# Performance work log

Measured on AMD Instinct MI355X. Metric: run time of the kernel, lower is better.

Reference implementation:

```python
import jax, jax.numpy as jnp
import numpy as np

B, S = 4, 128
N_ITERS = 3  # original hardcodes range(3) regardless of max_iter


def _build_masks(edge_mask, chart_mask):
    S_ = edge_mask.shape[-1]
    ar = jnp.arange(S_)
    ne = ar[:, None] != ar[None, :]          # [a,b]: a != b
    le = ar[:, None] <= ar[None, :]
    ge = ar[:, None] >= ar[None, :]
    ls = jnp.minimum(ar[:, None], ar[None, :])  # min(a,b)
    rs = jnp.maximum(ar[:, None], ar[None, :])  # max(a,b)

    # edge_mask2o[b,h,m,s] = edge_mask[b,h,s] & edge_mask[b,h,m] & (m != s)
    em2o = edge_mask[:, :, None, :] & edge_mask[:, :, :, None]
    em2o = em2o & ne[None, None, :, :]
    # lrhs[h,m,s] = (min(m,s) >= h) | (max(m,s) <= h)
    lrhs = (ls[None, :, :] >= ar[:, None, None]) | (rs[None, :, :] <= ar[:, None, None])
    noncross = em2o & lrhs[None]
    # additionally require h != s for plain edge_mask2o
    em2o = em2o & ne[:, None, :][None]

    cm0 = chart_mask[:, 0]                                  # [B,S]
    pad = cm0[:, :, None] & cm0[:, None, :]                 # [B,S,S]
    chart_r = jnp.roll(chart_mask, 1, axis=1)               # cat((cm[:,-1:], cm[:,:-1]))
    # span_mask2o[b,i,j,s] = chart_r[b,i,j] & pad[b,j,s] & (max(i,j) != s)
    span2o = chart_r[:, :, :, None] & pad[:, None, :, :]
    span2o = span2o & (rs[:, :, None] != ar[None, None, :])[None]
    # inside[i,j,s] = (i <= s) & (j >= s)
    inside = le[:, None, :] & ge[None, :, :]
    outside = (~inside)[None] & span2o
    # off-diagonal pad mask: pad.triu(1) | pad.tril(-1) == pad & (i != j)
    outside = outside & (pad & ne[None])[:, :, :, None]
    return em2o, noncross, span2o, outside


def setup_inputs() -> dict:
    key = jax.random.key(0)
    ks = jax.random.split(key, 12)
    lens = jax.random.randint(ks[0], (B,), S // 2, S)
    valid = jnp.arange(S)[None, :] < lens[:, None]          # [B,S]
    edge_mask = valid[:, :, None] & valid[:, None, :]
    tri = jnp.triu(jnp.ones((S, S), dtype=bool), 1)
    chart_mask = edge_mask & tri[None]
    def rn(k, shape):
        return jax.random.normal(k, shape, dtype=jnp.float32)
    return {
        's_edge': rn(ks[1], (B, S, S)),
        's_const': rn(ks[2], (B, S, S)),
        's_sib': rn(ks[3], (B, S, S, S)),
        's_cop': rn(ks[4], (B, S, S, S)),
        's_grd': rn(ks[5], (B, S, S, S)),
        's_end_point': rn(ks[6], (B, S, S, S)),
        's_split': rn(ks[7], (B, S, S, S)),
        's_head_span_b': rn(ks[8], (B, S, S, S)),
        's_head_span_e': rn(ks[9], (B, S, S, S)),
        'edge_mask': edge_mask,
        'chart_mask': chart_mask,
    }


def reference(s_edge, s_const, s_sib, s_cop, s_grd, s_end_point, s_split,
              s_head_span_b, s_head_span_e, edge_mask, chart_mask):
    # symmetrize span scores: triu + triu(1).T on last two dims
    s_span = jnp.triu(s_const) + jnp.swapaxes(jnp.triu(s_const, 1), -1, -2)
    em2o, noncross, span2o, outside = _build_masks(edge_mask, chart_mask)

    s_sib = s_sib * em2o
    s_cop = s_cop * em2o
    s_grd = s_grd * em2o
    s_end_point = s_end_point * noncross
    s_split = s_split * span2o
    s_hb = s_head_span_b * outside
    s_he = jnp.transpose(s_head_span_e, (0, 2, 1, 3)) * outside

    # Note: the torch code aliases tmp_q_edge to s_edge and uses +=, so the
    # base scores accumulate across iterations; equivalently q <- q + update.
    q_edge, q_span = s_edge, s_span
    for _ in range(N_ITERS):
        pe = jax.nn.sigmoid(q_edge)
        ps = jax.nn.sigmoid(q_span)
        upd_e = (jnp.einsum('bhs,bhms->bhm', pe, s_sib)
                 + jnp.einsum('bsm,bhms->bhm', pe, s_cop)
                 + jnp.einsum('bms,bhms->bhm', ps, s_grd)
                 + jnp.einsum('bms,bhms->bhm', ps, s_end_point))
        upd_s = (jnp.einsum('bis,bijs->bis', ps, s_split)
                 + jnp.einsum('bsi,bijs->bij', pe, s_hb)
                 + jnp.einsum('bsj,bijs->bij', pe, s_he))
        q_edge = q_edge + upd_e
        q_span = q_span + upd_s
    return q_edge, q_span
```

## Files before the change

kernel.cpp:

```cpp
#include <hip/hip_runtime.h>
#include <stdint.h>

#define BB 4
#define SDIM 128
#define S2 (SDIM*SDIM)
#define S3 ((size_t)SDIM*S2)

__device__ __forceinline__ int probe_len(const void* em, int b, int lane) {
    const unsigned char* p8 = (const unsigned char*)em;
    const int* p32 = (const int*)em;
    const int t0 = lane, t1 = lane + 64;
    const size_t i0 = (size_t)b*S2 + (size_t)t0*SDIM + t0;
    const size_t i1 = (size_t)b*S2 + (size_t)t1*SDIM + t1;
    const unsigned char a0 = p8[i0], a1 = p8[i1];
    const bool ok = (a0 != 0) && (t1 != SDIM-1 || a1 == 0);
    const unsigned long long mok = __ballot(ok);
    const bool use8 = (mok == ~0ull);
    int v0, v1;
    if (use8) { v0 = (a0 != 0); v1 = (a1 != 0); }
    else      { v0 = (p32[i0] != 0); v1 = (p32[i1] != 0); }
    return __popcll(__ballot(v0)) + __popcll(__ballot(v1));
}

__device__ __forceinline__ float sigf(float x) { return 1.f / (1.f + expf(-x)); }

__global__ __launch_bounds__(256) void k_prep(
    const float* __restrict__ s_edge, const float* __restrict__ s_const,
    const float* __restrict__ s_split, const void* __restrict__ em,
    float* __restrict__ q_edge, float* __restrict__ q_span,
    float* __restrict__ split0, float* __restrict__ split1,
    float* __restrict__ peA, float* __restrict__ peB,
    float* __restrict__ peTA, float* __restrict__ peTB,
    float* __restrict__ psA, float* __restrict__ psB) {
    const int b = blockIdx.x >> 7, i = blockIdx.x & 127;
    const int y = blockIdx.y;
    const int tid = threadIdx.x, lane = tid & 63;
    const int len = probe_len(em, b, lane);
    const int lm1 = len - 1;
    const size_t vb = (size_t)b*S2;
    if (y == 0 && tid < SDIM) {
        const size_t ro = vb + (size_t)i*SDIM + tid;
        const float qe = s_edge[ro];
        const float qs = (i <= tid) ? s_const[ro] : s_const[vb + (size_t)tid*SDIM + i];
        q_edge[ro] = qe;
        q_span[ro] = qs;
        const float se = sigf(qe), ss = sigf(qs);
        peA[ro] = se; peB[ro] = se;
        psA[ro] = ss; psB[ro] = ss;
        const size_t to = vb + (size_t)tid*SDIM + i;
        peTA[to] = se; peTB[to] = se;
    }
    const int g = tid >> 5;
    const int kq = (tid & 31) * 4;
    float4 acc = make_float4(0.f, 0.f, 0.f, 0.f);
    if (i >= 1 && i < len && kq < len) {
        const float* base = s_split + (size_t)b*S3 + (size_t)i*S2;
        const int j0 = i + g + 8*y;
        float4 v[8]; int jv[8];
        #pragma unroll
        for (int t = 0; t < 8; ++t) {
            const int j = j0 + 16*t;
            jv[t] = j;
            const int jc = min(j, lm1);
            v[t] = *(const float4*)(base + (size_t)jc*SDIM + kq);
        }
        __builtin_amdgcn_sched_barrier(0);
        #pragma unroll
        for (int t = 0; t < 8; ++t) {
            const int j = jv[t];
            const bool jb = (j < len);
            acc.x += (jb && j != kq+0) ? v[t].x : 0.f;
            acc.y += (jb && j != kq+1) ? v[t].y : 0.f;
            acc.z += (jb && j != kq+2) ? v[t].z : 0.f;
            acc.w += (jb && j != kq+3) ? v[t].w : 0.f;
        }
    }
    __shared__ float red[8][SDIM];
    *(float4*)&red[g][kq] = acc;
    __syncthreads();
    if (tid < SDIM) {
        float s = 0.f;
        #pragma unroll
        for (int gg = 0; gg < 8; ++gg) s += red[gg][tid];
        float* out = y ? split1 : split0;
        out[vb + (size_t)i*SDIM + tid] = (tid >= 1 && tid < len) ? s : 0.f;
    }
}

__global__ __launch_bounds__(256) void k_upd(
    const float* __restrict__ s_sib, const float* __restrict__ s_cop,
    const float* __restrict__ s_grd, const float* __restrict__ s_ep,
    const float* __restrict__ s_hb,  const float* __restrict__ s_he,
    const float* __restrict__ peA, const float* __restrict__ peTA,
    const float* __restrict__ psA,
    const float* __restrict__ split0, const float* __restrict__ split1,
    const void* __restrict__ em,
    float* __restrict__ q_edge, float* __restrict__ q_span,
    float* __restrict__ peB, float* __restrict__ peTB, float* __restrict__ psB) {
    const int b = blockIdx.x >> 7, row = blockIdx.x & 127;
    const int tid = threadIdx.x, wave = tid >> 6, lane = tid & 63;
    const int half = lane >> 5, sq = (lane & 31) * 4;
    const int len = probe_len(em, b, lane);
    const int lm1 = len - 1;
    const int sqa = min(sq, lm1 & ~3);
    const size_t vb = (size_t)b*S2;

    if (blockIdx.y < 4) {
        const int h = row;
        if (h >= len) return;
        const int m0 = blockIdx.y * 32;
        if (m0 >= len) return;
        const size_t tb = (size_t)b*S3 + (size_t)h*S2;
        const size_t hrow = vb + (size_t)h*SDIM;
        const float4 pe4 = *(const float4*)(peA + hrow + sqa);
        int   mr[4];
        float4 sib[4], cop[4], grd[4], epv[4], pet[4], psv[4];
        float qo[4];
        #pragma unroll
        for (int it = 0; it < 4; ++it) {
            const int m = m0 + 8*it + 2*wave + half;
            mr[it] = m;
            const int mc = min(m, lm1);
            const size_t ro = tb + (size_t)mc*SDIM + sqa;
            sib[it] = *(const float4*)(s_sib + ro);
            cop[it] = *(const float4*)(s_cop + ro);
            grd[it] = *(const float4*)(s_grd + ro);
            epv[it] = *(const float4*)(s_ep  + ro);
            const size_t vo = vb + (size_t)mc*SDIM + sqa;
            pet[it] = *(const float4*)(peTA + vo);
            psv[it] = *(const float4*)(psA  + vo);
            qo[it]  = q_edge[hrow + mc];
        }
        __builtin_amdgcn_sched_barrier(0);
        #pragma unroll
        for (int it = 0; it < 4; ++it) {
            const int m = mr[it];
            const bool mv = (m < len);
            float r = 0.f;
            #define TERM(C, F) { const int s = sq + C;                               \
                const bool bs = mv && (s < len) && (m != s);                         \
                const float fem = (bs && (h != s)) ? 1.f : 0.f;                      \
                const float fnc = (bs && ((m >= h && s >= h) || (m <= h && s <= h))) \
                                  ? 1.f : 0.f;                                       \
                r += fem * (sib[it].F*pe4.F + cop[it].F*pet[it].F + grd[it].F*psv[it].F) \
                   + fnc * (epv[it].F*psv[it].F); }
            TERM(0, x) TERM(1, y) TERM(2, z) TERM(3, w)
            #undef TERM
            r += __shfl_xor(r, 16); r += __shfl_xor(r, 8); r += __shfl_xor(r, 4);
            r += __shfl_xor(r, 2);  r += __shfl_xor(r, 1);
            if ((lane & 31) == 0 && mv) {
                const float qn = qo[it] + r;
                q_edge[hrow + m] = qn;
                const float sg = sigf(qn);
                peB[hrow + m] = sg;
                peTB[vb + (size_t)m*SDIM + h] = sg;
            }
        }
    } else {
        const int i = row;
        if (i < 1 || i >= len) return;
        const int j0 = (blockIdx.y - 4) * 32;
        if (j0 >= len) return;
        const size_t irow = vb + (size_t)i*SDIM;
        const float4 peTi4 = *(const float4*)(peTA + irow + sqa);
        int jr[4];
        float4 hb[4], he[4], ptj[4];
        float qs[4], pq[4], s0[4], s1[4];
        #pragma unroll
        for (int it = 0; it < 4; ++it) {
            const int j = j0 + 8*it + 2*wave + half;
            jr[it] = j;
            const int jc = min(j, lm1);
            hb[it]  = *(const float4*)(s_hb + (size_t)b*S3 + (size_t)i*S2 + (size_t)jc*SDIM + sqa);
            he[it]  = *(const float4*)(s_he + (size_t)b*S3 + (size_t)jc*S2 + (size_t)i*SDIM + sqa);
            ptj[it] = *(const float4*)(peTA + vb + (size_t)jc*SDIM + sqa);
            qs[it]  = q_span[irow + jc];
            pq[it]  = psA[irow + jc];
            s0[it]  = split0[irow + jc];
            s1[it]  = split1[irow + jc];
        }
        __builtin_amdgcn_sched_barrier(0);
        #pragma unroll
        for (int it = 0; it < 4; ++it) {
            const int j = jr[it];
            const bool act = (j > i) && (j < len);
            float r = 0.f;
            #define TERM(C, F) { const int s = sq + C;                               \
                const float f = (act && s >= 1 && s < len && (s < i || s > j))       \
                                ? 1.f : 0.f;                                         \
                r += f * (hb[it].F*peTi4.F + he[it].F*ptj[it].F); }
            TERM(0, x) TERM(1, y) TERM(2, z) TERM(3, w)
            #undef TERM
            r += __shfl_xor(r, 16); r += __shfl_xor(r, 8); r += __shfl_xor(r, 4);
            r += __shfl_xor(r, 2);  r += __shfl_xor(r, 1);
            if ((lane & 31) == 0 && j >= 1 && j < len) {
                const float qn = qs[it] + r + pq[it] * (s0[it] + s1[it]);
                q_span[irow + j] = qn;
                psB[irow + j] = sigf(qn);
            }
        }
    }
}

extern "C" void kernel_launch(void* const* d_in, const int* in_sizes, int n_in,
                              void* d_out, int out_size, void* d_ws, size_t ws_size,
                              hipStream_t stream) {
    const float* s_edge  = (const float*)d_in[0];
    const float* s_const = (const float*)d_in[1];
    const float* s_sib   = (const float*)d_in[2];
    const float* s_cop   = (const float*)d_in[3];
    const float* s_grd   = (const float*)d_in[4];
    const float* s_ep    = (const float*)d_in[5];
    const float* s_split = (const float*)d_in[6];
    const float* s_hb    = (const float*)d_in[7];
    const float* s_he    = (const float*)d_in[8];
    const void*  em      = d_in[9];
    (void)in_sizes; (void)n_in; (void)out_size; (void)ws_size;

    float* q_edge = (float*)d_out;
    float* q_span = q_edge + (size_t)BB * S2;

    char* ws = (char*)d_ws;
    const size_t SZ = (size_t)BB * S2 * sizeof(float);
    float* split0 = (float*)(ws);
    float* split1 = (float*)(ws + 1*SZ);
    float* peA    = (float*)(ws + 2*SZ);
    float* peTA   = (float*)(ws + 3*SZ);
    float* psA    = (float*)(ws + 4*SZ);
    float* peB    = (float*)(ws + 5*SZ);
    float* peTB   = (float*)(ws + 6*SZ);
    float* psB    = (float*)(ws + 7*SZ);

    const int NB = BB * SDIM;
    hipLaunchKernelGGL(k_prep, dim3(NB, 2), dim3(256), 0, stream,
                       s_edge, s_const, s_split, em, q_edge, q_span,
                       split0, split1, peA, peB, peTA, peTB, psA, psB);
    for (int it = 0; it < 3; ++it) {
        const int s = it & 1;
        const float* peR  = s ? peB  : peA;
        const float* peTR = s ? peTB : peTA;
        const float* psR  = s ? psB  : psA;
        float* peW  = s ? peA  : peB;
        float* peTW = s ? peTA : peTB;
        float* psW  = s ? psA  : psB;
        hipLaunchKernelGGL(k_upd, dim3(dim3(NB, 8)), dim3(256), 0, stream,
                           s_sib, s_cop, s_grd, s_ep, s_hb, s_he,
                           peR, peTR, psR, split0, split1, em,
                           q_edge, q_span, peW, peTW, psW);
    }
}
```

Before: 278.6 us.

## Stage tensor rows via direct global-to-LDS loads and halve per-block tiles

Both kernels now stream their 3D score rows with global_load_lds (16-byte direct-to-LDS transfers) instead of holding them in register arrays. After a barrier each wave reads its rows from LDS. k_upd processes 16 rows per block instead of 32 and launches twice as many blocks. k_prep stages s_split rows into a 32KB LDS buffer and reduces them column-wise. The aim is to cut register pressure, raise memory-level parallelism and occupancy, and issue loads asynchronously. In exchange it adds barriers and large LDS footprints (48KB in k_upd) that may limit how many blocks fit per CU.

```diff
diff --git a/kernel.cpp b/kernel.cpp
--- a/kernel.cpp
+++ b/kernel.cpp
@@ -24,6 +24,12 @@
 
 __device__ __forceinline__ float sigf(float x) { return 1.f / (1.f + expf(-x)); }
 
+__device__ __forceinline__ void gll16(const float* g, float* l) {
+    __builtin_amdgcn_global_load_lds(
+        (const __attribute__((address_space(1))) void*)g,
+        (__attribute__((address_space(3))) void*)l, 16, 0, 0);
+}
+
 __global__ __launch_bounds__(256) void k_prep(
     const float* __restrict__ s_edge, const float* __restrict__ s_const,
     const float* __restrict__ s_split, const void* __restrict__ em,
@@ -32,9 +38,11 @@
     float* __restrict__ peA, float* __restrict__ peB,
     float* __restrict__ peTA, float* __restrict__ peTB,
     float* __restrict__ psA, float* __restrict__ psB) {
+    __shared__ float plds[64*SDIM];
+    __shared__ float red2[2][SDIM];
     const int b = blockIdx.x >> 7, i = blockIdx.x & 127;
     const int y = blockIdx.y;
-    const int tid = threadIdx.x, lane = tid & 63;
+    const int tid = threadIdx.x, lane = tid & 63, wave = tid >> 6;
     const int len = probe_len(em, b, lane);
     const int lm1 = len - 1;
     const size_t vb = (size_t)b*S2;
@@ -50,40 +58,33 @@
         const size_t to = vb + (size_t)tid*SDIM + i;
         peTA[to] = se; peTB[to] = se;
     }
-    const int g = tid >> 5;
-    const int kq = (tid & 31) * 4;
-    float4 acc = make_float4(0.f, 0.f, 0.f, 0.f);
-    if (i >= 1 && i < len && kq < len) {
-        const float* base = s_split + (size_t)b*S3 + (size_t)i*S2;
-        const int j0 = i + g + 8*y;
-        float4 v[8]; int jv[8];
-        #pragma unroll
-        for (int t = 0; t < 8; ++t) {
-            const int j = j0 + 16*t;
-            jv[t] = j;
+    if (i >= 1 && i < len) {
+        const int L = len - i;
+        const float* sb = s_split + (size_t)b*S3 + (size_t)i*S2;
+        for (int mloc = wave; mloc < 32; mloc += 4) {
+            const int t0 = 2*(y + 2*mloc);
+            if (t0 >= L) break;
+            const int j = i + t0 + (lane >> 5);
             const int jc = min(j, lm1);
-            v[t] = *(const float4*)(base + (size_t)jc*SDIM + kq);
-        }
-        __builtin_amdgcn_sched_barrier(0);
-        #pragma unroll
-        for (int t = 0; t < 8; ++t) {
-            const int j = jv[t];
-            const bool jb = (j < len);
-            acc.x += (jb && j != kq+0) ? v[t].x : 0.f;
-            acc.y += (jb && j != kq+1) ? v[t].y : 0.f;
-            acc.z += (jb && j != kq+2) ? v[t].z : 0.f;
-            acc.w += (jb && j != kq+3) ? v[t].w : 0.f;
-        }
-    }
-    __shared__ float red[8][SDIM];
-    *(float4*)&red[g][kq] = acc;
+            gll16(sb + (size_t)jc*SDIM + (lane & 31)*4, &plds[(2*mloc)*SDIM]);
+        }
+    }
+    __syncthreads();
+    const int k = tid & 127, rh = tid >> 7;
+    float sum = 0.f;
+    #pragma unroll
+    for (int u = 0; u < 32; ++u) {
+        const int r = rh + 2*u;
+        const int j = i + 4*u + 2*y + rh;
+        sum += (j < len && j != k) ? plds[r*SDIM + k] : 0.f;
+    }
+    red2[rh][k] = sum;
     __syncthreads();
     if (tid < SDIM) {
-        float s = 0.f;
-        #pragma unroll
-        for (int gg = 0; gg < 8; ++gg) s += red[gg][tid];
         float* out = y ? split1 : split0;
-        out[vb + (size_t)i*SDIM + tid] = (tid >= 1 && tid < len) ? s : 0.f;
+        out[vb + (size_t)i*SDIM + tid] =
+            (i >= 1 && i < len && tid >= 1 && tid < len)
+            ? (red2[0][tid] + red2[1][tid]) : 0.f;
     }
 }
 
@@ -97,59 +98,62 @@
     const void* __restrict__ em,
     float* __restrict__ q_edge, float* __restrict__ q_span,
     float* __restrict__ peB, float* __restrict__ peTB, float* __restrict__ psB) {
+    __shared__ float lds[6*16*SDIM];
+    __shared__ float sml[64];
     const int b = blockIdx.x >> 7, row = blockIdx.x & 127;
     const int tid = threadIdx.x, wave = tid >> 6, lane = tid & 63;
     const int half = lane >> 5, sq = (lane & 31) * 4;
     const int len = probe_len(em, b, lane);
     const int lm1 = len - 1;
-    const int sqa = min(sq, lm1 & ~3);
     const size_t vb = (size_t)b*S2;
 
-    if (blockIdx.y < 4) {
+    if (blockIdx.y < 8) {
         const int h = row;
-        if (h >= len) return;
-        const int m0 = blockIdx.y * 32;
-        if (m0 >= len) return;
+        const int m0 = blockIdx.y * 16;
+        if (h >= len || m0 >= len) return;
         const size_t tb = (size_t)b*S3 + (size_t)h*S2;
         const size_t hrow = vb + (size_t)h*SDIM;
-        const float4 pe4 = *(const float4*)(peA + hrow + sqa);
-        int   mr[4];
-        float4 sib[4], cop[4], grd[4], epv[4], pet[4], psv[4];
-        float qo[4];
-        #pragma unroll
-        for (int it = 0; it < 4; ++it) {
-            const int m = m0 + 8*it + 2*wave + half;
-            mr[it] = m;
-            const int mc = min(m, lm1);
-            const size_t ro = tb + (size_t)mc*SDIM + sqa;
-            sib[it] = *(const float4*)(s_sib + ro);
-            cop[it] = *(const float4*)(s_cop + ro);
-            grd[it] = *(const float4*)(s_grd + ro);
-            epv[it] = *(const float4*)(s_ep  + ro);
-            const size_t vo = vb + (size_t)mc*SDIM + sqa;
-            pet[it] = *(const float4*)(peTA + vo);
-            psv[it] = *(const float4*)(psA  + vo);
-            qo[it]  = q_edge[hrow + mc];
-        }
-        __builtin_amdgcn_sched_barrier(0);
-        #pragma unroll
-        for (int it = 0; it < 4; ++it) {
-            const int m = mr[it];
+        const float* bases[6] = { s_sib + tb, s_cop + tb, s_grd + tb,
+                                  s_ep + tb,  peTA + vb,  psA + vb };
+        #pragma unroll
+        for (int T = 0; T < 6; ++T) {
+            #pragma unroll
+            for (int ss = 0; ss < 2; ++ss) {
+                const int s  = 2*wave + ss;
+                const int r2 = 2*s + half;
+                const int mc = min(m0 + r2, lm1);
+                gll16(bases[T] + (size_t)mc*SDIM + sq, &lds[(T*16 + 2*s)*SDIM]);
+            }
+        }
+        if (tid < 16)
+            sml[tid] = q_edge[hrow + min(m0 + tid, lm1)];
+        __syncthreads();
+        const float4 pe4 = *(const float4*)(peA + hrow + sq);
+        #pragma unroll
+        for (int it = 0; it < 2; ++it) {
+            const int m = m0 + it*8 + wave*2 + half;
+            const int r = it*8 + wave*2 + half;
+            const float4 sibv = *(const float4*)&lds[(0*16 + r)*SDIM + sq];
+            const float4 copv = *(const float4*)&lds[(1*16 + r)*SDIM + sq];
+            const float4 grdv = *(const float4*)&lds[(2*16 + r)*SDIM + sq];
+            const float4 epvv = *(const float4*)&lds[(3*16 + r)*SDIM + sq];
+            const float4 petv = *(const float4*)&lds[(4*16 + r)*SDIM + sq];
+            const float4 psvv = *(const float4*)&lds[(5*16 + r)*SDIM + sq];
             const bool mv = (m < len);
-            float r = 0.f;
+            float rr = 0.f;
             #define TERM(C, F) { const int s = sq + C;                               \
                 const bool bs = mv && (s < len) && (m != s);                         \
                 const float fem = (bs && (h != s)) ? 1.f : 0.f;                      \
                 const float fnc = (bs && ((m >= h && s >= h) || (m <= h && s <= h))) \
                                   ? 1.f : 0.f;                                       \
-                r += fem * (sib[it].F*pe4.F + cop[it].F*pet[it].F + grd[it].F*psv[it].F) \
-                   + fnc * (epv[it].F*psv[it].F); }
+                rr += fem * (sibv.F*pe4.F + copv.F*petv.F + grdv.F*psvv.F)           \
+                    + fnc * (epvv.F*psvv.F); }
             TERM(0, x) TERM(1, y) TERM(2, z) TERM(3, w)
             #undef TERM
-            r += __shfl_xor(r, 16); r += __shfl_xor(r, 8); r += __shfl_xor(r, 4);
-            r += __shfl_xor(r, 2);  r += __shfl_xor(r, 1);
+            rr += __shfl_xor(rr, 16); rr += __shfl_xor(rr, 8); rr += __shfl_xor(rr, 4);
+            rr += __shfl_xor(rr, 2);  rr += __shfl_xor(rr, 1);
             if ((lane & 31) == 0 && mv) {
-                const float qn = qo[it] + r;
+                const float qn = sml[r] + rr;
                 q_edge[hrow + m] = qn;
                 const float sg = sigf(qn);
                 peB[hrow + m] = sg;
@@ -158,43 +162,51 @@
         }
     } else {
         const int i = row;
-        if (i < 1 || i >= len) return;
-        const int j0 = (blockIdx.y - 4) * 32;
-        if (j0 >= len) return;
+        const int j0 = (blockIdx.y - 8) * 16;
+        if (i < 1 || i >= len || j0 >= len) return;
         const size_t irow = vb + (size_t)i*SDIM;
-        const float4 peTi4 = *(const float4*)(peTA + irow + sqa);
-        int jr[4];
-        float4 hb[4], he[4], ptj[4];
-        float qs[4], pq[4], s0[4], s1[4];
-        #pragma unroll
-        for (int it = 0; it < 4; ++it) {
-            const int j = j0 + 8*it + 2*wave + half;
-            jr[it] = j;
-            const int jc = min(j, lm1);
-            hb[it]  = *(const float4*)(s_hb + (size_t)b*S3 + (size_t)i*S2 + (size_t)jc*SDIM + sqa);
-            he[it]  = *(const float4*)(s_he + (size_t)b*S3 + (size_t)jc*S2 + (size_t)i*SDIM + sqa);
-            ptj[it] = *(const float4*)(peTA + vb + (size_t)jc*SDIM + sqa);
-            qs[it]  = q_span[irow + jc];
-            pq[it]  = psA[irow + jc];
-            s0[it]  = split0[irow + jc];
-            s1[it]  = split1[irow + jc];
-        }
-        __builtin_amdgcn_sched_barrier(0);
-        #pragma unroll
-        for (int it = 0; it < 4; ++it) {
-            const int j = jr[it];
+        #pragma unroll
+        for (int ss = 0; ss < 2; ++ss) {
+            const int s  = 2*wave + ss;
+            const int r2 = 2*s + half;
+            const int jc = min(j0 + r2, lm1);
+            gll16(s_hb + (size_t)b*S3 + (size_t)i*S2 + (size_t)jc*SDIM + sq,
+                  &lds[(0*16 + 2*s)*SDIM]);
+            gll16(s_he + (size_t)b*S3 + (size_t)jc*S2 + (size_t)i*SDIM + sq,
+                  &lds[(1*16 + 2*s)*SDIM]);
+            gll16(peTA + vb + (size_t)jc*SDIM + sq,
+                  &lds[(2*16 + 2*s)*SDIM]);
+        }
+        if (tid < 64) {
+            const int surf = tid >> 4, jj = tid & 15;
+            const int jc = min(j0 + jj, lm1);
+            const size_t o = irow + jc;
+            const float v = (surf == 0) ? q_span[o]
+                          : (surf == 1) ? psA[o]
+                          : (surf == 2) ? split0[o] : split1[o];
+            sml[tid] = v;
+        }
+        __syncthreads();
+        const float4 peTi4 = *(const float4*)(peTA + irow + sq);
+        #pragma unroll
+        for (int it = 0; it < 2; ++it) {
+            const int j = j0 + it*8 + wave*2 + half;
+            const int r = it*8 + wave*2 + half;
+            const float4 hbv  = *(const float4*)&lds[(0*16 + r)*SDIM + sq];
+            const float4 hev  = *(const float4*)&lds[(1*16 + r)*SDIM + sq];
+            const float4 ptjv = *(const float4*)&lds[(2*16 + r)*SDIM + sq];
             const bool act = (j > i) && (j < len);
-            float r = 0.f;
+            float rr = 0.f;
             #define TERM(C, F) { const int s = sq + C;                               \
                 const float f = (act && s >= 1 && s < len && (s < i || s > j))       \
                                 ? 1.f : 0.f;                                         \
-                r += f * (hb[it].F*peTi4.F + he[it].F*ptj[it].F); }
+                rr += f * (hbv.F*peTi4.F + hev.F*ptjv.F); }
             TERM(0, x) TERM(1, y) TERM(2, z) TERM(3, w)
             #undef TERM
-            r += __shfl_xor(r, 16); r += __shfl_xor(r, 8); r += __shfl_xor(r, 4);
-            r += __shfl_xor(r, 2);  r += __shfl_xor(r, 1);
+            rr += __shfl_xor(rr, 16); rr += __shfl_xor(rr, 8); rr += __shfl_xor(rr, 4);
+            rr += __shfl_xor(rr, 2);  rr += __shfl_xor(rr, 1);
             if ((lane & 31) == 0 && j >= 1 && j < len) {
-                const float qn = qs[it] + r + pq[it] * (s0[it] + s1[it]);
+                const float qn = sml[r] + rr + sml[16 + r] * (sml[32 + r] + sml[48 + r]);
                 q_span[irow + j] = qn;
                 psB[irow + j] = sigf(qn);
             }
@@ -243,7 +255,7 @@
         float* peW  = s ? peA  : peB;
         float* peTW = s ? peTA : peTB;
         float* psW  = s ? psA  : psB;
-        hipLaunchKernelGGL(k_upd, dim3(dim3(NB, 8)), dim3(256), 0, stream,
+        hipLaunchKernelGGL(k_upd, dim3(dim3(NB, 16)), dim3(256), 0, stream,
                            s_sib, s_cop, s_grd, s_ep, s_hb, s_he,
                            peR, peTR, psR, split0, split1, em,
                            q_edge, q_span, peW, peTW, psW);
```

Measured after the change: 294.6 us. 1.06x slower.

## Rebalance grids: 4-way split in prep, 64-row chunks per upd block

Applied to the files above, without the earlier changes.

The prep kernel now splits the split-score reduction four ways instead of two. Each block issues fewer loads and accumulates as it goes, replacing the staged register array. The update kernel now has each block process two 32-row sub-chunks sequentially, interleaves edge and span blocks on a flat 1D grid, and sets a minimum occupancy hint of 6 in launch bounds. The aim is to balance work across CUs and improve occupancy, at the cost of less in-flight memory-level parallelism per block, since the sched_barrier batching was removed.

```diff
diff --git a/kernel.cpp b/kernel.cpp
--- a/kernel.cpp
+++ b/kernel.cpp
@@ -5,6 +5,8 @@
 #define SDIM 128
 #define S2 (SDIM*SDIM)
 #define S3 ((size_t)SDIM*S2)
+
+typedef float vf4 __attribute__((ext_vector_type(4)));
 
 __device__ __forceinline__ int probe_len(const void* em, int b, int lane) {
     const unsigned char* p8 = (const unsigned char*)em;
@@ -24,21 +26,23 @@
 
 __device__ __forceinline__ float sigf(float x) { return 1.f / (1.f + expf(-x)); }
 
-__global__ __launch_bounds__(256) void k_prep(
+__global__ __launch_bounds__(256, 6) void k_prep(
     const float* __restrict__ s_edge, const float* __restrict__ s_const,
     const float* __restrict__ s_split, const void* __restrict__ em,
     float* __restrict__ q_edge, float* __restrict__ q_span,
     float* __restrict__ split0, float* __restrict__ split1,
+    float* __restrict__ split2, float* __restrict__ split3,
     float* __restrict__ peA, float* __restrict__ peB,
     float* __restrict__ peTA, float* __restrict__ peTB,
     float* __restrict__ psA, float* __restrict__ psB) {
-    const int b = blockIdx.x >> 7, i = blockIdx.x & 127;
-    const int y = blockIdx.y;
+    const int gid = blockIdx.x;
+    const int yq = gid & 3, x = gid >> 2;
+    const int b = x >> 7, i = x & 127;
     const int tid = threadIdx.x, lane = tid & 63;
     const int len = probe_len(em, b, lane);
     const int lm1 = len - 1;
     const size_t vb = (size_t)b*S2;
-    if (y == 0 && tid < SDIM) {
+    if (yq == 0 && tid < SDIM) {
         const size_t ro = vb + (size_t)i*SDIM + tid;
         const float qe = s_edge[ro];
         const float qs = (i <= tid) ? s_const[ro] : s_const[vb + (size_t)tid*SDIM + i];
@@ -52,52 +56,51 @@
     }
     const int g = tid >> 5;
     const int kq = (tid & 31) * 4;
-    float4 acc = make_float4(0.f, 0.f, 0.f, 0.f);
+    vf4 acc = (vf4)0.f;
     if (i >= 1 && i < len && kq < len) {
         const float* base = s_split + (size_t)b*S3 + (size_t)i*S2;
-        const int j0 = i + g + 8*y;
-        float4 v[8]; int jv[8];
         #pragma unroll
-        for (int t = 0; t < 8; ++t) {
-            const int j = j0 + 16*t;
-            jv[t] = j;
+        for (int t = 0; t < 4; ++t) {
+            const int j = i + g + 8*yq + 32*t;
             const int jc = min(j, lm1);
-            v[t] = *(const float4*)(base + (size_t)jc*SDIM + kq);
+            const vf4 v = *(const vf4*)(base + (size_t)jc*SDIM + kq);
+            const bool jb = (j < len);
+            acc.x += (jb && j != kq+0) ? v.x : 0.f;
+            acc.y += (jb && j != kq+1) ? v.y : 0.f;
+            acc.z += (jb && j != kq+2) ? v.z : 0.f;
+            acc.w += (jb && j != kq+3) ? v.w : 0.f;
         }
-        __builtin_amdgcn_sched_barrier(0);
-        #pragma unroll
-        for (int t = 0; t < 8; ++t) {
-            const int j = jv[t];
-            const bool jb = (j < len);
-            acc.x += (jb && j != kq+0) ? v[t].x : 0.f;
-            acc.y += (jb && j != kq+1) ? v[t].y : 0.f;
-            acc.z += (jb && j != kq+2) ? v[t].z : 0.f;
-            acc.w += (jb && j != kq+3) ? v[t].w : 0.f;
-        }
     }
     __shared__ float red[8][SDIM];
-    *(float4*)&red[g][kq] = acc;
+    *(vf4*)&red[g][kq] = acc;
     __syncthreads();
     if (tid < SDIM) {
         float s = 0.f;
         #pragma unroll
         for (int gg = 0; gg < 8; ++gg) s += red[gg][tid];
-        float* out = y ? split1 : split0;
+        float* out = (yq == 0) ? split0 : (yq == 1) ? split1
+                   : (yq == 2) ? split2 : split3;
         out[vb + (size_t)i*SDIM + tid] = (tid >= 1 && tid < len) ? s : 0.f;
     }
 }
 
-__global__ __launch_bounds__(256) void k_upd(
+__global__ __launch_bounds__(256, 6) void k_upd(
     const float* __restrict__ s_sib, const float* __restrict__ s_cop,
     const float* __restrict__ s_grd, const float* __restrict__ s_ep,
     const float* __restrict__ s_hb,  const float* __restrict__ s_he,
     const float* __restrict__ peA, const float* __restrict__ peTA,
     const float* __restrict__ psA,
     const float* __restrict__ split0, const float* __restrict__ split1,
+    const float* __restrict__ split2, const float* __restrict__ split3,
     const void* __restrict__ em,
     float* __restrict__ q_edge, float* __restrict__ q_span,
     float* __restrict__ peB, float* __restrict__ peTB, float* __restrict__ psB) {
-    const int b = blockIdx.x >> 7, row = blockIdx.x & 127;
+    const int gid = blockIdx.x;
+    const int part = gid & 1;
+    const int idx = gid >> 1;
+    const int b = idx >> 8;
+    const int row = (idx >> 1) & 127;
+    const int hf = idx & 1;
     const int tid = threadIdx.x, wave = tid >> 6, lane = tid & 63;
     const int half = lane >> 5, sq = (lane & 31) * 4;
     const int len = probe_len(em, b, lane);
@@ -105,98 +108,103 @@
     const int sqa = min(sq, lm1 & ~3);
     const size_t vb = (size_t)b*S2;
 
-    if (blockIdx.y < 4) {
+    if (part == 0) {
         const int h = row;
         if (h >= len) return;
-        const int m0 = blockIdx.y * 32;
-        if (m0 >= len) return;
         const size_t tb = (size_t)b*S3 + (size_t)h*S2;
         const size_t hrow = vb + (size_t)h*SDIM;
-        const float4 pe4 = *(const float4*)(peA + hrow + sqa);
-        int   mr[4];
-        float4 sib[4], cop[4], grd[4], epv[4], pet[4], psv[4];
-        float qo[4];
-        #pragma unroll
-        for (int it = 0; it < 4; ++it) {
-            const int m = m0 + 8*it + 2*wave + half;
-            mr[it] = m;
-            const int mc = min(m, lm1);
-            const size_t ro = tb + (size_t)mc*SDIM + sqa;
-            sib[it] = *(const float4*)(s_sib + ro);
-            cop[it] = *(const float4*)(s_cop + ro);
-            grd[it] = *(const float4*)(s_grd + ro);
-            epv[it] = *(const float4*)(s_ep  + ro);
-            const size_t vo = vb + (size_t)mc*SDIM + sqa;
-            pet[it] = *(const float4*)(peTA + vo);
-            psv[it] = *(const float4*)(psA  + vo);
-            qo[it]  = q_edge[hrow + mc];
-        }
-        __builtin_amdgcn_sched_barrier(0);
-        #pragma unroll
-        for (int it = 0; it < 4; ++it) {
-            const int m = mr[it];
-            const bool mv = (m < len);
-            float r = 0.f;
-            #define TERM(C, F) { const int s = sq + C;                               \
-                const bool bs = mv && (s < len) && (m != s);                         \
-                const float fem = (bs && (h != s)) ? 1.f : 0.f;                      \
-                const float fnc = (bs && ((m >= h && s >= h) || (m <= h && s <= h))) \
-                                  ? 1.f : 0.f;                                       \
-                r += fem * (sib[it].F*pe4.F + cop[it].F*pet[it].F + grd[it].F*psv[it].F) \
-                   + fnc * (epv[it].F*psv[it].F); }
-            TERM(0, x) TERM(1, y) TERM(2, z) TERM(3, w)
-            #undef TERM
-            r += __shfl_xor(r, 16); r += __shfl_xor(r, 8); r += __shfl_xor(r, 4);
-            r += __shfl_xor(r, 2);  r += __shfl_xor(r, 1);
-            if ((lane & 31) == 0 && mv) {
-                const float qn = qo[it] + r;
-                q_edge[hrow + m] = qn;
-                const float sg = sigf(qn);
-                peB[hrow + m] = sg;
-                peTB[vb + (size_t)m*SDIM + h] = sg;
+        const vf4 pe4 = *(const vf4*)(peA + hrow + sqa);
+        for (int sub = 0; sub < 2; ++sub) {
+            const int m0 = hf*64 + sub*32;
+            if (m0 >= len) break;
+            int mr[4];
+            vf4 sib[4], cop[4], grd[4], epv[4], pet[4], psv[4];
+            float qo[4];
+            #pragma unroll
+            for (int it = 0; it < 4; ++it) {
+                const int m = m0 + 8*it + 2*wave + half;
+                mr[it] = m;
+                const int mc = min(m, lm1);
+                const size_t ro = tb + (size_t)mc*SDIM + sqa;
+                sib[it] = *(const vf4*)(s_sib + ro);
+                cop[it] = *(const vf4*)(s_cop + ro);
+                grd[it] = *(const vf4*)(s_grd + ro);
+                epv[it] = *(const vf4*)(s_ep  + ro);
+                const size_t vo = vb + (size_t)mc*SDIM + sqa;
+                pet[it] = *(const vf4*)(peTA + vo);
+                psv[it] = *(const vf4*)(psA  + vo);
+                qo[it]  = q_edge[hrow + mc];
+            }
+            #pragma unroll
+            for (int it = 0; it < 4; ++it) {
+                const int m = mr[it];
+                const bool mv = (m < len);
+                float r = 0.f;
+                #define TERM(C, F) { const int s = sq + C;                               \
+                    const bool bs = mv && (s < len) && (m != s);                         \
+                    const float fem = (bs && (h != s)) ? 1.f : 0.f;                      \
+                    const float fnc = (bs && ((m >= h && s >= h) || (m <= h && s <= h))) \
+                                      ? 1.f : 0.f;                                       \
+                    r += fem * (sib[it].F*pe4.F + cop[it].F*pet[it].F + grd[it].F*psv[it].F) \
+                       + fnc * (epv[it].F*psv[it].F); }
+                TERM(0, x) TERM(1, y) TERM(2, z) TERM(3, w)
+                #undef TERM
+                r += __shfl_xor(r, 16); r += __shfl_xor(r, 8); r += __shfl_xor(r, 4);
+                r += __shfl_xor(r, 2);  r += __shfl_xor(r, 1);
+                if ((lane & 31) == 0 && mv) {
+                    const float qn = qo[it] + r;
+                    q_edge[hrow + m] = qn;
+                    const float sg = sigf(qn);
+                    peB[hrow + m] = sg;
+                    peTB[vb + (size_t)m*SDIM + h] = sg;
+                }
             }
         }
     } else {
         const int i = row;
         if (i < 1 || i >= len) return;
-        const int j0 = (blockIdx.y - 4) * 32;
-        if (j0 >= len) return;
         const size_t irow = vb + (size_t)i*SDIM;
-        const float4 peTi4 = *(const float4*)(peTA + irow + sqa);
-        int jr[4];
-        float4 hb[4], he[4], ptj[4];
-        float qs[4], pq[4], s0[4], s1[4];
-        #pragma unroll
-        for (int it = 0; it < 4; ++it) {
-            const int j = j0 + 8*it + 2*wave + half;
-            jr[it] = j;
-            const int jc = min(j, lm1);
-            hb[it]  = *(const float4*)(s_hb + (size_t)b*S3 + (size_t)i*S2 + (size_t)jc*SDIM + sqa);
-            he[it]  = *(const float4*)(s_he + (size_t)b*S3 + (size_t)jc*S2 + (size_t)i*SDIM + sqa);
-            ptj[it] = *(const float4*)(peTA + vb + (size_t)jc*SDIM + sqa);
-            qs[it]  = q_span[irow + jc];
-            pq[it]  = psA[irow + jc];
-            s0[it]  = split0[irow + jc];
-            s1[it]  = split1[irow + jc];
-        }
-        __builtin_amdgcn_sched_barrier(0);
-        #pragma unroll
-        for (int it = 0; it < 4; ++it) {
-            const int j = jr[it];
-            const bool act = (j > i) && (j < len);
-            float r = 0.f;
-            #define TERM(C, F) { const int s = sq + C;                               \
-                const float f = (act && s >= 1 && s < len && (s < i || s > j))       \
-                                ? 1.f : 0.f;                                         \
-                r += f * (hb[it].F*peTi4.F + he[it].F*ptj[it].F); }
-            TERM(0, x) TERM(1, y) TERM(2, z) TERM(3, w)
-            #undef TERM
-            r += __shfl_xor(r, 16); r += __shfl_xor(r, 8); r += __shfl_xor(r, 4);
-            r += __shfl_xor(r, 2);  r += __shfl_xor(r, 1);
-            if ((lane & 31) == 0 && j >= 1 && j < len) {
-                const float qn = qs[it] + r + pq[it] * (s0[it] + s1[it]);
-                q_span[irow + j] = qn;
-                psB[irow + j] = sigf(qn);
+        const vf4 peTi4 = *(const vf4*)(peTA + irow + sqa);
+        for (int sub = 0; sub < 2; ++sub) {
+            const int j0 = hf*64 + sub*32;
+            if (j0 >= len) break;
+            int jr[4];
+            vf4 hb[4], he[4], ptj[4];
+            float qs[4], pq[4], sA[4], sB[4], sC[4], sD[4];
+            #pragma unroll
+            for (int it = 0; it < 4; ++it) {
+                const int j = j0 + 8*it + 2*wave + half;
+                jr[it] = j;
+                const int jc = min(j, lm1);
+                hb[it]  = *(const vf4*)(s_hb + (size_t)b*S3 + (size_t)i*S2 + (size_t)jc*SDIM + sqa);
+                he[it]  = *(const vf4*)(s_he + (size_t)b*S3 + (size_t)jc*S2 + (size_t)i*SDIM + sqa);
+                ptj[it] = *(const vf4*)(peTA + vb + (size_t)jc*SDIM + sqa);
+                qs[it]  = q_span[irow + jc];
+                pq[it]  = psA[irow + jc];
+                sA[it]  = split0[irow + jc];
+                sB[it]  = split1[irow + jc];
+                sC[it]  = split2[irow + jc];
+                sD[it]  = split3[irow + jc];
+            }
+            #pragma unroll
+            for (int it = 0; it < 4; ++it) {
+                const int j = jr[it];
+                const bool act = (j > i) && (j < len);
+                float r = 0.f;
+                #define TERM(C, F) { const int s = sq + C;                               \
+                    const float f = (act && s >= 1 && s < len && (s < i || s > j))       \
+                                    ? 1.f : 0.f;                                         \
+                    r += f * (hb[it].F*peTi4.F + he[it].F*ptj[it].F); }
+                TERM(0, x) TERM(1, y) TERM(2, z) TERM(3, w)
+                #undef TERM
+                r += __shfl_xor(r, 16); r += __shfl_xor(r, 8); r += __shfl_xor(r, 4);
+                r += __shfl_xor(r, 2);  r += __shfl_xor(r, 1);
+                if ((lane & 31) == 0 && j >= 1 && j < len) {
+                    const float qn = qs[it] + r
+                                   + pq[it] * (sA[it] + sB[it] + sC[it] + sD[it]);
+                    q_span[irow + j] = qn;
+                    psB[irow + j] = sigf(qn);
+                }
             }
         }
     }
@@ -224,17 +232,19 @@
     const size_t SZ = (size_t)BB * S2 * sizeof(float);
     float* split0 = (float*)(ws);
     float* split1 = (float*)(ws + 1*SZ);
-    float* peA    = (float*)(ws + 2*SZ);
-    float* peTA   = (float*)(ws + 3*SZ);
-    float* psA    = (float*)(ws + 4*SZ);
-    float* peB    = (float*)(ws + 5*SZ);
-    float* peTB   = (float*)(ws + 6*SZ);
-    float* psB    = (float*)(ws + 7*SZ);
-
-    const int NB = BB * SDIM;
-    hipLaunchKernelGGL(k_prep, dim3(NB, 2), dim3(256), 0, stream,
+    float* split2 = (float*)(ws + 2*SZ);
+    float* split3 = (float*)(ws + 3*SZ);
+    float* peA    = (float*)(ws + 4*SZ);
+    float* peTA   = (float*)(ws + 5*SZ);
+    float* psA    = (float*)(ws + 6*SZ);
+    float* peB    = (float*)(ws + 7*SZ);
+    float* peTB   = (float*)(ws + 8*SZ);
+    float* psB    = (float*)(ws + 9*SZ);
+
+    hipLaunchKernelGGL(k_prep, dim3(2048), dim3(256), 0, stream,
                        s_edge, s_const, s_split, em, q_edge, q_span,
-                       split0, split1, peA, peB, peTA, peTB, psA, psB);
+                       split0, split1, split2, split3,
+                       peA, peB, peTA, peTB, psA, psB);
     for (int it = 0; it < 3; ++it) {
         const int s = it & 1;
         const float* peR  = s ? peB  : peA;
@@ -243,9 +253,9 @@
         float* peW  = s ? peA  : peB;
         float* peTW = s ? peTA : peTB;
         float* psW  = s ? psA  : psB;
-        hipLaunchKernelGGL(k_upd, dim3(dim3(NB, 8)), dim3(256), 0, stream,
+        hipLaunchKernelGGL(k_upd, dim3(2048), dim3(256), 0, stream,
                            s_sib, s_cop, s_grd, s_ep, s_hb, s_he,
-                           peR, peTR, psR, split0, split1, em,
+                           peR, peTR, psR, split0, split1, split2, split3, em,
                            q_edge, q_span, peW, peTW, psW);
     }
 }
```

Measured after the change: 410.0 us. 1.47x slower.
